# Kernel tuning notes

Hardware: AMD Instinct MI355X
Metric: run time of the kernel (lower is better)

Reference implementation:

```python
import jax, jax.numpy as jnp
import numpy as np

N_MAPS = 6          # n: maps per class (5 kernels + 1 text)
N_CLASSES = 2       # len(text_classify)
RATIO = 3
LAMBDA = 0.7
EPS = 1e-4
NEG_INF = -1e30


def setup_inputs() -> dict:
    key = jax.random.key(0)
    k1, k2, k3 = jax.random.split(key, 3)
    B, C, H, W = 8, N_CLASSES * N_MAPS, 640, 640
    outputs = jax.random.normal(k1, (B, C, H, W), dtype=jnp.float32)
    labels = jax.random.uniform(k2, (B, C, H, W), dtype=jnp.float32)
    training_mask = jax.random.uniform(k3, (B, 1, H, W), dtype=jnp.float32)
    return {"outputs": outputs, "labels": labels, "training_mask": training_mask}


def _dice_loss(pred, target, mask):
    # pred/target: (B, HW) or (B, K, HW); mask broadcastable. sums over last axis.
    p = jax.nn.sigmoid(pred) * mask
    t = target * mask
    a = jnp.sum(p * t, axis=-1)
    b = jnp.sum(p * p, axis=-1) + EPS
    c = jnp.sum(t * t, axis=-1) + EPS
    return 1.0 - 2.0 * a / (b + c)


def _ohem_single(score, gt, tm):
    # score/gt/tm: (H, W). Returns float32 (H, W) selection mask.
    pos_num = jnp.sum((gt > 0.5) & (tm > 0.5))
    neg = gt <= 0.5
    neg_total = jnp.sum(neg)
    neg_num = jnp.minimum(pos_num * RATIO, neg_total)
    # descending sort of negative-position scores
    neg_sorted = -jnp.sort(-jnp.where(neg, score, NEG_INF).ravel())
    thr = neg_sorted[jnp.clip(neg_num - 1, 0, score.size - 1)]
    sel = ((score >= thr) | (gt > 0.5)) & (tm > 0.5)
    fallback = (pos_num == 0) | (neg_num == 0)
    return jnp.where(fallback, tm, sel.astype(jnp.float32))


def reference(outputs, labels, training_mask):
    B, C, H, W = outputs.shape
    tm = training_mask[:, 0]  # (B, H, W)
    text_losses, kernel_losses, class_losses = [], [], []
    for i in range(N_CLASSES):
        texts = outputs[:, (i + 1) * N_MAPS - 1]                 # (B, H, W)
        kernels = outputs[:, i * N_MAPS:(i + 1) * N_MAPS - 1]    # (B, K, H, W)
        gt_texts = labels[:, (i + 1) * N_MAPS - 1]
        gt_kernels = labels[:, i * N_MAPS:(i + 1) * N_MAPS - 1]
        # OHEM mask (detached in original via numpy round-trip)
        sel_text = jax.lax.stop_gradient(jax.vmap(_ohem_single)(texts, gt_texts, tm))
        loss_text = _dice_loss(texts.reshape(B, -1), gt_texts.reshape(B, -1),
                               sel_text.reshape(B, -1))  # (B,)
        # kernel mask: (sigmoid(texts) > 0.5) & (tm > 0.5), detached
        sel_k = jax.lax.stop_gradient(
            ((jax.nn.sigmoid(texts) > 0.5) & (tm > 0.5)).astype(jnp.float32))
        K = gt_kernels.shape[1]
        loss_kernels = _dice_loss(kernels.reshape(B, K, -1),
                                  gt_kernels.reshape(B, K, -1),
                                  sel_k.reshape(B, 1, -1))  # (B, K) per-kernel losses
        loss_kernels = jnp.mean(loss_kernels, axis=1)  # mean over kernels -> (B,)
        lt = jnp.mean(loss_text)      # reduction='mean'
        lk = jnp.mean(loss_kernels)
        loss = LAMBDA * lt + (1.0 - LAMBDA) * lk
        text_losses.append(lt)
        kernel_losses.append(lk)
        class_losses.append(loss)
    muti_class_loss_avg = jnp.mean(jnp.stack(class_losses))
    text_loss_avg = jnp.mean(jnp.stack(text_losses))
    kernel_loss_avg = jnp.mean(jnp.stack(kernel_losses))
    # stacked as (3,): [muti_class_loss_avg, text_loss_avg, kernel_loss_avg]
    return jnp.stack([muti_class_loss_avg, text_loss_avg, kernel_loss_avg])
```

## Files before the change

### kernel.cpp

```cpp
#include <hip/hip_runtime.h>
#include <hip/hip_cooperative_groups.h>
namespace cg = cooperative_groups;

#define HW 409600
#define NCH 12

#define OFF_TACC   0
#define OFF_KACC   256
#define OFF_TFAST  1280
#define OFF_TFB    1536
#define OFF_POSF   1792
#define OFF_NEGF   1856
#define OFF_DONE   1920
#define OFF_NEGNUM 1984
#define OFF_SEL1   2048
#define OFF_KREM1  2112
#define OFF_SEL2   2176
#define OFF_KREM2  2240
#define OFF_THR    2304
#define OFF_ANYG   2368
#define OFF_HA     4096
#define OFF_HB     (OFF_HA + 16*2048*4)
#define OFF_HC     (OFF_HB + 16*2048*4)

__device__ __forceinline__ unsigned flipkey(float x){
  unsigned b = __float_as_uint(x);
  return (b & 0x80000000u) ? ~b : (b | 0x80000000u);
}
__device__ __forceinline__ float unflip(unsigned u){
  unsigned b = (u & 0x80000000u) ? (u ^ 0x80000000u) : ~u;
  return __uint_as_float(b);
}
__device__ __forceinline__ float sigm(float x){
  return __fdividef(1.0f, 1.0f + __expf(-x));
}

__global__ __launch_bounds__(256) void k_main(
    const float* __restrict__ outputs, const float* __restrict__ labels,
    const float* __restrict__ tmask,
    float* __restrict__ posF, float* __restrict__ negF,
    float* __restrict__ tfastA, float* __restrict__ tfbA,
    float* __restrict__ kaccA)
{
  int img = blockIdx.x / 400;
  int blk = blockIdx.x % 400;
  int ci = img >> 3, bi = img & 7;
  const float* ob = outputs + (size_t)(bi*NCH + ci*6)*HW;
  const float* lb = labels  + (size_t)(bi*NCH + ci*6)*HW;
  const float* mp = tmask   + (size_t)bi*HW;
  int px = blk*1024 + (int)threadIdx.x*4;

  float4 ov0 = *(const float4*)(ob + 0*HW + px);
  float4 ov1 = *(const float4*)(ob + 1*HW + px);
  float4 ov2 = *(const float4*)(ob + 2*HW + px);
  float4 ov3 = *(const float4*)(ob + 3*HW + px);
  float4 ov4 = *(const float4*)(ob + 4*HW + px);
  float4 ov5 = *(const float4*)(ob + 5*HW + px);
  float4 lv0 = *(const float4*)(lb + 0*HW + px);
  float4 lv1 = *(const float4*)(lb + 1*HW + px);
  float4 lv2 = *(const float4*)(lb + 2*HW + px);
  float4 lv3 = *(const float4*)(lb + 3*HW + px);
  float4 lv4 = *(const float4*)(lb + 4*HW + px);
  float4 lv5 = *(const float4*)(lb + 5*HW + px);
  float4 mv  = *(const float4*)(mp + px);

  float oo[6][4] = {{ov0.x,ov0.y,ov0.z,ov0.w},{ov1.x,ov1.y,ov1.z,ov1.w},
                    {ov2.x,ov2.y,ov2.z,ov2.w},{ov3.x,ov3.y,ov3.z,ov3.w},
                    {ov4.x,ov4.y,ov4.z,ov4.w},{ov5.x,ov5.y,ov5.z,ov5.w}};
  float ll[6][4] = {{lv0.x,lv0.y,lv0.z,lv0.w},{lv1.x,lv1.y,lv1.z,lv1.w},
                    {lv2.x,lv2.y,lv2.z,lv2.w},{lv3.x,lv3.y,lv3.z,lv3.w},
                    {lv4.x,lv4.y,lv4.z,lv4.w},{lv5.x,lv5.y,lv5.z,lv5.w}};
  float tmv[4] = {mv.x,mv.y,mv.z,mv.w};

  float ka0=0,ka1=0,ka2=0,ka3=0,ka4=0;
  float kb0=0,kb1=0,kb2=0,kb3=0,kb4=0;
  float kc0=0,kc1=0,kc2=0,kc3=0,kc4=0;
  float af=0,bf=0,cf=0;
  float ab_=0,bb_=0,cb_=0;
  unsigned pos=0, neg=0;

  #pragma unroll
  for (int c=0;c<4;c++){
    float t  = oo[5][c];
    float g  = ll[5][c];
    float tm = tmv[c];
    bool tpos  = (tm > 0.5f);
    bool isneg = (g <= 0.5f);
    bool selk  = (t > 0.0f) && tpos;
    pos += (unsigned)((!isneg) && tpos);
    neg += (unsigned)isneg;

    float s5 = sigm(t);
    float mf = tpos ? 1.0f : 0.0f;
    af += mf * (s5*g);
    bf += mf * (s5*s5);
    cf += mf * (g*g);
    float pfb = s5*tm, tfb = g*tm;
    ab_ += pfb*tfb; bb_ += pfb*pfb; cb_ += tfb*tfb;
    float mk = selk ? 1.0f : 0.0f;
    {
      float s, l;
      s = sigm(oo[0][c]); l = ll[0][c];
      ka0 += mk*(s*l); kb0 += mk*(s*s); kc0 += mk*(l*l);
      s = sigm(oo[1][c]); l = ll[1][c];
      ka1 += mk*(s*l); kb1 += mk*(s*s); kc1 += mk*(l*l);
      s = sigm(oo[2][c]); l = ll[2][c];
      ka2 += mk*(s*l); kb2 += mk*(s*s); kc2 += mk*(l*l);
      s = sigm(oo[3][c]); l = ll[3][c];
      ka3 += mk*(s*l); kb3 += mk*(s*s); kc3 += mk*(l*l);
      s = sigm(oo[4][c]); l = ll[4][c];
      ka4 += mk*(s*l); kb4 += mk*(s*s); kc4 += mk*(l*l);
    }
  }

  float red[23] = {af,bf,cf, ab_,bb_,cb_,
                   ka0,kb0,kc0, ka1,kb1,kc1, ka2,kb2,kc2,
                   ka3,kb3,kc3, ka4,kb4,kc4,
                   (float)pos, (float)neg};
  #pragma unroll
  for (int k=0;k<23;k++){
    #pragma unroll
    for (int o=32;o;o>>=1) red[k] += __shfl_down(red[k],o,64);
  }
  __shared__ float sred[4][23];
  int wv = threadIdx.x >> 6, ln = threadIdx.x & 63;
  if (ln==0){
    #pragma unroll
    for (int k=0;k<23;k++) sred[wv][k] = red[k];
  }
  __syncthreads();
  int t = threadIdx.x;
  if (t < 23){
    float v = sred[0][t]+sred[1][t]+sred[2][t]+sred[3][t];
    float* dst;
    if      (t < 3)  dst = tfastA + img*3 + t;
    else if (t < 6)  dst = tfbA   + img*3 + (t-3);
    else if (t < 21) dst = kaccA  + img*15 + (t-6);
    else if (t ==21) dst = posF + img;
    else             dst = negF + img;
    atomicAdd(dst, v);
  }
}

template<int NB>
__device__ void scan_desc(const unsigned* h, unsigned k, unsigned* selOut, unsigned* kremOut)
{
  const int PER = NB/256;
  int t = threadIdx.x;
  unsigned s=0;
  #pragma unroll
  for (int j=0;j<PER;j++) s += h[t*PER+j];
  __shared__ unsigned cs[256];
  cs[t]=s; __syncthreads();
  if (t==0){
    unsigned cum=0, ch=0, kin=k;
    for (int c=255;c>=0;c--){
      if (cum + cs[c] >= k){ ch=(unsigned)c; kin=k-cum; break; }
      cum += cs[c];
    }
    unsigned cum2=0, sel=ch*PER, kr=1;
    for (int x=PER-1;x>=0;x--){
      unsigned v = h[ch*PER+x];
      cum2 += v;
      if (cum2 >= kin){ sel=ch*PER+(unsigned)x; kr = kin - (cum2 - v); break; }
    }
    *selOut = sel; *kremOut = kr;
  }
  __syncthreads();
}

__device__ void do_final(const float* tacc, const float* kacc, float* out)
{
  const float EPSF = 1e-4f;
  float ltA[2], lkA[2];
  for (int i=0;i<2;i++){
    float lt=0.f;
    for (int b=0;b<8;b++){
      int img=i*8+b;
      float a=tacc[img*3], p2=tacc[img*3+1]+EPSF, t2=tacc[img*3+2]+EPSF;
      lt += 1.f - 2.f*a/(p2+t2);
    }
    lt *= 0.125f;
    float lk=0.f;
    for (int b=0;b<8;b++) for (int k=0;k<5;k++){
      int idx=((i*8+b)*5+k)*3;
      float a=kacc[idx], p2=kacc[idx+1]+EPSF, t2=kacc[idx+2]+EPSF;
      lk += 1.f - 2.f*a/(p2+t2);
    }
    lk /= 40.f;
    ltA[i]=lt; lkA[i]=lk;
  }
  float l0 = 0.7f*ltA[0] + 0.3f*lkA[0];
  float l1 = 0.7f*ltA[1] + 0.3f*lkA[1];
  out[0]=0.5f*(l0+l1);
  out[1]=0.5f*(ltA[0]+ltA[1]);
  out[2]=0.5f*(lkA[0]+lkA[1]);
}

__global__ __launch_bounds__(256) void k_tail(
    const float* __restrict__ outputs, const float* __restrict__ labels,
    const float* __restrict__ tmask, char* __restrict__ ws, float* __restrict__ out)
{
  cg::grid_group grid = cg::this_grid();
  float* tacc      = (float*)(ws + OFF_TACC);
  float* kacc      = (float*)(ws + OFF_KACC);
  float* tfastA    = (float*)(ws + OFF_TFAST);
  float* tfbA      = (float*)(ws + OFF_TFB);
  float* posF      = (float*)(ws + OFF_POSF);
  float* negF      = (float*)(ws + OFF_NEGF);
  unsigned* doneA  = (unsigned*)(ws + OFF_DONE);
  unsigned* negnumA= (unsigned*)(ws + OFF_NEGNUM);
  unsigned* sel1A  = (unsigned*)(ws + OFF_SEL1);
  unsigned* krem1A = (unsigned*)(ws + OFF_KREM1);
  unsigned* sel2A  = (unsigned*)(ws + OFF_SEL2);
  unsigned* krem2A = (unsigned*)(ws + OFF_KREM2);
  float* thrA      = (float*)(ws + OFF_THR);
  unsigned* anyG   = (unsigned*)(ws + OFF_ANYG);
  unsigned* histA  = (unsigned*)(ws + OFF_HA);
  unsigned* histB  = (unsigned*)(ws + OFF_HB);
  unsigned* histC  = (unsigned*)(ws + OFF_HC);

  if (blockIdx.x == 0){
    int t = threadIdx.x;
    unsigned d = 1u;
    if (t < 16){
      float pos = posF[t], negt = negF[t];
      float nn = fminf(pos*3.0f, negt);
      bool fb   = (pos == 0.0f) || (nn == 0.0f);
      bool fast = (!fb) && (nn == negt);
      d = (fb || fast) ? 1u : 0u;
      doneA[t] = d;
      negnumA[t] = d ? 1u : (unsigned)(nn + 0.5f);
      thrA[t] = 0.0f;
      if (d){
        const float* src = fb ? (tfbA + t*3) : (tfastA + t*3);
        tacc[t*3+0] = src[0];
        tacc[t*3+1] = src[1];
        tacc[t*3+2] = src[2];
      }
    }
    unsigned long long nd = __ballot((t < 16) && (d == 0u));
    if (t == 0) anyG[0] = (nd != 0ull) ? 1u : 0u;
    __threadfence();
  }
  grid.sync();

  if (anyG[0] == 0u){
    if (blockIdx.x == 0 && threadIdx.x == 0) do_final(tacc, kacc, out);
    return;
  }

  for (int i = blockIdx.x*256 + threadIdx.x; i < 81920; i += gridDim.x*256)
    histA[i] = 0u;
  grid.sync();

  __shared__ unsigned lh[2048];

  for (int tile = blockIdx.x; tile < 800; tile += gridDim.x){
    int img = tile/50;
    if (doneA[img]) continue;
    int blk = tile%50;
    int ci = img>>3, bi = img&7;
    const float* tp = outputs + (size_t)(bi*NCH + ci*6 + 5)*HW;
    const float* gp = labels  + (size_t)(bi*NCH + ci*6 + 5)*HW;
    for (int j=threadIdx.x; j<2048; j+=256) lh[j]=0u;
    __syncthreads();
    for (int it=0; it<8; it++){
      int px = blk*8192 + it*1024 + (int)threadIdx.x*4;
      float4 tv = *(const float4*)(tp+px);
      float4 gv = *(const float4*)(gp+px);
      float tt[4]={tv.x,tv.y,tv.z,tv.w};
      float gg[4]={gv.x,gv.y,gv.z,gv.w};
      #pragma unroll
      for (int c=0;c<4;c++)
        if (gg[c] <= 0.5f) atomicAdd(&lh[flipkey(tt[c]) >> 21], 1u);
    }
    __syncthreads();
    unsigned* gh = histA + (size_t)img*2048u;
    for (int j=threadIdx.x; j<2048; j+=256){
      unsigned v = lh[j];
      if (v) atomicAdd(&gh[j], v);
    }
    __syncthreads();
  }
  grid.sync();

  if (blockIdx.x < 16 && !doneA[blockIdx.x])
    scan_desc<2048>(histA + (size_t)blockIdx.x*2048u, negnumA[blockIdx.x],
                    &sel1A[blockIdx.x], &krem1A[blockIdx.x]);
  grid.sync();

  for (int tile = blockIdx.x; tile < 800; tile += gridDim.x){
    int img = tile/50;
    if (doneA[img]) continue;
    int blk = tile%50;
    int ci = img>>3, bi = img&7;
    unsigned sel1 = sel1A[img];
    const float* tp = outputs + (size_t)(bi*NCH + ci*6 + 5)*HW;
    const float* gp = labels  + (size_t)(bi*NCH + ci*6 + 5)*HW;
    for (int j=threadIdx.x; j<2048; j+=256) lh[j]=0u;
    __syncthreads();
    for (int it=0; it<8; it++){
      int px = blk*8192 + it*1024 + (int)threadIdx.x*4;
      float4 tv = *(const float4*)(tp+px);
      float4 gv = *(const float4*)(gp+px);
      float tt[4]={tv.x,tv.y,tv.z,tv.w};
      float gg[4]={gv.x,gv.y,gv.z,gv.w};
      #pragma unroll
      for (int c=0;c<4;c++){
        if (gg[c] <= 0.5f){
          unsigned key = flipkey(tt[c]);
          if ((key>>21) == sel1) atomicAdd(&lh[(key>>10) & 0x7FFu], 1u);
        }
      }
    }
    __syncthreads();
    unsigned* gh = histB + (size_t)img*2048u;
    for (int j=threadIdx.x; j<2048; j+=256){
      unsigned v = lh[j];
      if (v) atomicAdd(&gh[j], v);
    }
    __syncthreads();
  }
  grid.sync();

  if (blockIdx.x < 16 && !doneA[blockIdx.x])
    scan_desc<2048>(histB + (size_t)blockIdx.x*2048u, krem1A[blockIdx.x],
                    &sel2A[blockIdx.x], &krem2A[blockIdx.x]);
  grid.sync();

  for (int tile = blockIdx.x; tile < 800; tile += gridDim.x){
    int img = tile/50;
    if (doneA[img]) continue;
    int blk = tile%50;
    int ci = img>>3, bi = img&7;
    unsigned p22 = (sel1A[img]<<11) | sel2A[img];
    const float* tp = outputs + (size_t)(bi*NCH + ci*6 + 5)*HW;
    const float* gp = labels  + (size_t)(bi*NCH + ci*6 + 5)*HW;
    for (int j=threadIdx.x; j<1024; j+=256) lh[j]=0u;
    __syncthreads();
    for (int it=0; it<8; it++){
      int px = blk*8192 + it*1024 + (int)threadIdx.x*4;
      float4 tv = *(const float4*)(tp+px);
      float4 gv = *(const float4*)(gp+px);
      float tt[4]={tv.x,tv.y,tv.z,tv.w};
      float gg[4]={gv.x,gv.y,gv.z,gv.w};
      #pragma unroll
      for (int c=0;c<4;c++){
        if (gg[c] <= 0.5f){
          unsigned key = flipkey(tt[c]);
          if ((key>>10) == p22) atomicAdd(&lh[key & 0x3FFu], 1u);
        }
      }
    }
    __syncthreads();
    unsigned* gh = histC + (size_t)img*1024u;
    for (int j=threadIdx.x; j<1024; j+=256){
      unsigned v = lh[j];
      if (v) atomicAdd(&gh[j], v);
    }
    __syncthreads();
  }
  grid.sync();

  if (blockIdx.x < 16 && !doneA[blockIdx.x]){
    __shared__ unsigned sel3, kr;
    scan_desc<1024>(histC + (size_t)blockIdx.x*1024u, krem2A[blockIdx.x], &sel3, &kr);
    if (threadIdx.x==0){
      unsigned key = (sel1A[blockIdx.x]<<21) | (sel2A[blockIdx.x]<<10) | sel3;
      thrA[blockIdx.x] = unflip(key);
    }
  }
  grid.sync();

  for (int tile = blockIdx.x; tile < 800; tile += gridDim.x){
    int img = tile/50;
    if (doneA[img]) continue;
    int blk = tile%50;
    int ci = img>>3, bi = img&7;
    const float* tp = outputs + (size_t)(bi*NCH + ci*6 + 5)*HW;
    const float* gp = labels  + (size_t)(bi*NCH + ci*6 + 5)*HW;
    const float* mp = tmask   + (size_t)bi*HW;
    float thr = thrA[img];
    float sa=0.f, sb=0.f, sc=0.f;
    for (int it=0; it<8; it++){
      int px = blk*8192 + it*1024 + (int)threadIdx.x*4;
      float4 pv = *(const float4*)(tp+px);
      float4 gv = *(const float4*)(gp+px);
      float4 mv = *(const float4*)(mp+px);
      float pa[4]={pv.x,pv.y,pv.z,pv.w};
      float ga[4]={gv.x,gv.y,gv.z,gv.w};
      float ma[4]={mv.x,mv.y,mv.z,mv.w};
      #pragma unroll
      for (int c=0;c<4;c++){
        float m = (((pa[c] >= thr) || (ga[c] > 0.5f)) && (ma[c] > 0.5f)) ? 1.0f : 0.0f;
        float p = sigm(pa[c]) * m;
        float tt = ga[c]*m;
        sa += p*tt; sb += p*p; sc += tt*tt;
      }
    }
    #pragma unroll
    for (int o=32;o;o>>=1){
      sa += __shfl_down(sa,o,64); sb += __shfl_down(sb,o,64); sc += __shfl_down(sc,o,64);
    }
    __shared__ float ra[4], rb[4], rc[4];
    int wv = threadIdx.x>>6, ln = threadIdx.x&63;
    if (ln==0){ ra[wv]=sa; rb[wv]=sb; rc[wv]=sc; }
    __syncthreads();
    if (threadIdx.x==0){
      float* acc = tacc + img*3;
      atomicAdd(acc+0, ra[0]+ra[1]+ra[2]+ra[3]);
      atomicAdd(acc+1, rb[0]+rb[1]+rb[2]+rb[3]);
      atomicAdd(acc+2, rc[0]+rc[1]+rc[2]+rc[3]);
    }
    __syncthreads();
  }
  grid.sync();

  if (blockIdx.x == 0 && threadIdx.x == 0) do_final(tacc, kacc, out);
}

extern "C" void kernel_launch(void* const* d_in, const int* in_sizes, int n_in,
                              void* d_out, int out_size, void* d_ws, size_t ws_size,
                              hipStream_t stream)
{
  const float* outputs = (const float*)d_in[0];
  const float* labels  = (const float*)d_in[1];
  const float* tmask   = (const float*)d_in[2];
  float* out = (float*)d_out;
  char* ws = (char*)d_ws;
  float* posF      = (float*)(ws + OFF_POSF);
  float* negF      = (float*)(ws + OFF_NEGF);
  float* tfastA    = (float*)(ws + OFF_TFAST);
  float* tfbA      = (float*)(ws + OFF_TFB);
  float* kacc      = (float*)(ws + OFF_KACC);

  hipMemsetAsync(ws, 0, 2048, stream);
  k_main<<<6400,256,0,stream>>>(outputs, labels, tmask, posF, negF,
                                tfastA, tfbA, kacc);
  void* args[] = { (void*)&outputs, (void*)&labels, (void*)&tmask,
                   (void*)&ws, (void*)&out };
  hipLaunchCooperativeKernel((const void*)k_tail, dim3(256), dim3(256),
                             args, 0, stream);
}
```

Baseline: 392.9 us.

## Replace cooperative grid-synced tail with per-image block and partial-slot reduction

```diff
diff --git a/kernel.cpp b/kernel.cpp
--- a/kernel.cpp
+++ b/kernel.cpp
@@ -1,27 +1,12 @@
 #include <hip/hip_runtime.h>
-#include <hip/hip_cooperative_groups.h>
-namespace cg = cooperative_groups;
 
 #define HW 409600
 #define NCH 12
 
-#define OFF_TACC   0
-#define OFF_KACC   256
-#define OFF_TFAST  1280
-#define OFF_TFB    1536
-#define OFF_POSF   1792
-#define OFF_NEGF   1856
-#define OFF_DONE   1920
-#define OFF_NEGNUM 1984
-#define OFF_SEL1   2048
-#define OFF_KREM1  2112
-#define OFF_SEL2   2176
-#define OFF_KREM2  2240
-#define OFF_THR    2304
-#define OFF_ANYG   2368
-#define OFF_HA     4096
-#define OFF_HB     (OFF_HA + 16*2048*4)
-#define OFF_HC     (OFF_HB + 16*2048*4)
+#define OFF_PSLOT  0
+#define OFF_TACC   294912
+#define OFF_KACC   295168
+#define OFF_CNT    296192
 
 __device__ __forceinline__ unsigned flipkey(float x){
   unsigned b = __float_as_uint(x);
@@ -37,40 +22,16 @@
 
 __global__ __launch_bounds__(256) void k_main(
     const float* __restrict__ outputs, const float* __restrict__ labels,
-    const float* __restrict__ tmask,
-    float* __restrict__ posF, float* __restrict__ negF,
-    float* __restrict__ tfastA, float* __restrict__ tfbA,
-    float* __restrict__ kaccA)
-{
-  int img = blockIdx.x / 400;
-  int blk = blockIdx.x % 400;
+    const float* __restrict__ tmask, float* __restrict__ pslot,
+    unsigned* __restrict__ cnt)
+{
+  if (blockIdx.x == 0 && threadIdx.x == 0) *cnt = 0u;
+  int img = blockIdx.x / 200;
+  int blk = blockIdx.x % 200;
   int ci = img >> 3, bi = img & 7;
   const float* ob = outputs + (size_t)(bi*NCH + ci*6)*HW;
   const float* lb = labels  + (size_t)(bi*NCH + ci*6)*HW;
   const float* mp = tmask   + (size_t)bi*HW;
-  int px = blk*1024 + (int)threadIdx.x*4;
-
-  float4 ov0 = *(const float4*)(ob + 0*HW + px);
-  float4 ov1 = *(const float4*)(ob + 1*HW + px);
-  float4 ov2 = *(const float4*)(ob + 2*HW + px);
-  float4 ov3 = *(const float4*)(ob + 3*HW + px);
-  float4 ov4 = *(const float4*)(ob + 4*HW + px);
-  float4 ov5 = *(const float4*)(ob + 5*HW + px);
-  float4 lv0 = *(const float4*)(lb + 0*HW + px);
-  float4 lv1 = *(const float4*)(lb + 1*HW + px);
-  float4 lv2 = *(const float4*)(lb + 2*HW + px);
-  float4 lv3 = *(const float4*)(lb + 3*HW + px);
-  float4 lv4 = *(const float4*)(lb + 4*HW + px);
-  float4 lv5 = *(const float4*)(lb + 5*HW + px);
-  float4 mv  = *(const float4*)(mp + px);
-
-  float oo[6][4] = {{ov0.x,ov0.y,ov0.z,ov0.w},{ov1.x,ov1.y,ov1.z,ov1.w},
-                    {ov2.x,ov2.y,ov2.z,ov2.w},{ov3.x,ov3.y,ov3.z,ov3.w},
-                    {ov4.x,ov4.y,ov4.z,ov4.w},{ov5.x,ov5.y,ov5.z,ov5.w}};
-  float ll[6][4] = {{lv0.x,lv0.y,lv0.z,lv0.w},{lv1.x,lv1.y,lv1.z,lv1.w},
-                    {lv2.x,lv2.y,lv2.z,lv2.w},{lv3.x,lv3.y,lv3.z,lv3.w},
-                    {lv4.x,lv4.y,lv4.z,lv4.w},{lv5.x,lv5.y,lv5.z,lv5.w}};
-  float tmv[4] = {mv.x,mv.y,mv.z,mv.w};
 
   float ka0=0,ka1=0,ka2=0,ka3=0,ka4=0;
   float kb0=0,kb1=0,kb2=0,kb3=0,kb4=0;
@@ -80,36 +41,62 @@
   unsigned pos=0, neg=0;
 
   #pragma unroll
-  for (int c=0;c<4;c++){
-    float t  = oo[5][c];
-    float g  = ll[5][c];
-    float tm = tmv[c];
-    bool tpos  = (tm > 0.5f);
-    bool isneg = (g <= 0.5f);
-    bool selk  = (t > 0.0f) && tpos;
-    pos += (unsigned)((!isneg) && tpos);
-    neg += (unsigned)isneg;
-
-    float s5 = sigm(t);
-    float mf = tpos ? 1.0f : 0.0f;
-    af += mf * (s5*g);
-    bf += mf * (s5*s5);
-    cf += mf * (g*g);
-    float pfb = s5*tm, tfb = g*tm;
-    ab_ += pfb*tfb; bb_ += pfb*pfb; cb_ += tfb*tfb;
-    float mk = selk ? 1.0f : 0.0f;
-    {
-      float s, l;
-      s = sigm(oo[0][c]); l = ll[0][c];
-      ka0 += mk*(s*l); kb0 += mk*(s*s); kc0 += mk*(l*l);
-      s = sigm(oo[1][c]); l = ll[1][c];
-      ka1 += mk*(s*l); kb1 += mk*(s*s); kc1 += mk*(l*l);
-      s = sigm(oo[2][c]); l = ll[2][c];
-      ka2 += mk*(s*l); kb2 += mk*(s*s); kc2 += mk*(l*l);
-      s = sigm(oo[3][c]); l = ll[3][c];
-      ka3 += mk*(s*l); kb3 += mk*(s*s); kc3 += mk*(l*l);
-      s = sigm(oo[4][c]); l = ll[4][c];
-      ka4 += mk*(s*l); kb4 += mk*(s*s); kc4 += mk*(l*l);
+  for (int it=0; it<2; it++){
+    int px = blk*2048 + it*1024 + (int)threadIdx.x*4;
+    float4 ov0 = *(const float4*)(ob + 0*HW + px);
+    float4 ov1 = *(const float4*)(ob + 1*HW + px);
+    float4 ov2 = *(const float4*)(ob + 2*HW + px);
+    float4 ov3 = *(const float4*)(ob + 3*HW + px);
+    float4 ov4 = *(const float4*)(ob + 4*HW + px);
+    float4 ov5 = *(const float4*)(ob + 5*HW + px);
+    float4 lv0 = *(const float4*)(lb + 0*HW + px);
+    float4 lv1 = *(const float4*)(lb + 1*HW + px);
+    float4 lv2 = *(const float4*)(lb + 2*HW + px);
+    float4 lv3 = *(const float4*)(lb + 3*HW + px);
+    float4 lv4 = *(const float4*)(lb + 4*HW + px);
+    float4 lv5 = *(const float4*)(lb + 5*HW + px);
+    float4 mv  = *(const float4*)(mp + px);
+
+    float oo[6][4] = {{ov0.x,ov0.y,ov0.z,ov0.w},{ov1.x,ov1.y,ov1.z,ov1.w},
+                      {ov2.x,ov2.y,ov2.z,ov2.w},{ov3.x,ov3.y,ov3.z,ov3.w},
+                      {ov4.x,ov4.y,ov4.z,ov4.w},{ov5.x,ov5.y,ov5.z,ov5.w}};
+    float ll[6][4] = {{lv0.x,lv0.y,lv0.z,lv0.w},{lv1.x,lv1.y,lv1.z,lv1.w},
+                      {lv2.x,lv2.y,lv2.z,lv2.w},{lv3.x,lv3.y,lv3.z,lv3.w},
+                      {lv4.x,lv4.y,lv4.z,lv4.w},{lv5.x,lv5.y,lv5.z,lv5.w}};
+    float tmv[4] = {mv.x,mv.y,mv.z,mv.w};
+
+    #pragma unroll
+    for (int c=0;c<4;c++){
+      float t  = oo[5][c];
+      float g  = ll[5][c];
+      float tm = tmv[c];
+      bool tpos  = (tm > 0.5f);
+      bool isneg = (g <= 0.5f);
+      bool selk  = (t > 0.0f) && tpos;
+      pos += (unsigned)((!isneg) && tpos);
+      neg += (unsigned)isneg;
+
+      float s5 = sigm(t);
+      float mf = tpos ? 1.0f : 0.0f;
+      af += mf * (s5*g);
+      bf += mf * (s5*s5);
+      cf += mf * (g*g);
+      float pfb = s5*tm, tfb = g*tm;
+      ab_ += pfb*tfb; bb_ += pfb*pfb; cb_ += tfb*tfb;
+      float mk = selk ? 1.0f : 0.0f;
+      {
+        float s, l;
+        s = sigm(oo[0][c]); l = ll[0][c];
+        ka0 += mk*(s*l); kb0 += mk*(s*s); kc0 += mk*(l*l);
+        s = sigm(oo[1][c]); l = ll[1][c];
+        ka1 += mk*(s*l); kb1 += mk*(s*s); kc1 += mk*(l*l);
+        s = sigm(oo[2][c]); l = ll[2][c];
+        ka2 += mk*(s*l); kb2 += mk*(s*s); kc2 += mk*(l*l);
+        s = sigm(oo[3][c]); l = ll[3][c];
+        ka3 += mk*(s*l); kb3 += mk*(s*s); kc3 += mk*(l*l);
+        s = sigm(oo[4][c]); l = ll[4][c];
+        ka4 += mk*(s*l); kb4 += mk*(s*s); kc4 += mk*(l*l);
+      }
     }
   }
 
@@ -130,16 +117,8 @@
   }
   __syncthreads();
   int t = threadIdx.x;
-  if (t < 23){
-    float v = sred[0][t]+sred[1][t]+sred[2][t]+sred[3][t];
-    float* dst;
-    if      (t < 3)  dst = tfastA + img*3 + t;
-    else if (t < 6)  dst = tfbA   + img*3 + (t-3);
-    else if (t < 21) dst = kaccA  + img*15 + (t-6);
-    else if (t ==21) dst = posF + img;
-    else             dst = negF + img;
-    atomicAdd(dst, v);
-  }
+  if (t < 23)
+    pslot[(size_t)blockIdx.x*23 + t] = sred[0][t]+sred[1][t]+sred[2][t]+sred[3][t];
 }
 
 template<int NB>
@@ -201,190 +180,114 @@
     const float* __restrict__ outputs, const float* __restrict__ labels,
     const float* __restrict__ tmask, char* __restrict__ ws, float* __restrict__ out)
 {
-  cg::grid_group grid = cg::this_grid();
-  float* tacc      = (float*)(ws + OFF_TACC);
-  float* kacc      = (float*)(ws + OFF_KACC);
-  float* tfastA    = (float*)(ws + OFF_TFAST);
-  float* tfbA      = (float*)(ws + OFF_TFB);
-  float* posF      = (float*)(ws + OFF_POSF);
-  float* negF      = (float*)(ws + OFF_NEGF);
-  unsigned* doneA  = (unsigned*)(ws + OFF_DONE);
-  unsigned* negnumA= (unsigned*)(ws + OFF_NEGNUM);
-  unsigned* sel1A  = (unsigned*)(ws + OFF_SEL1);
-  unsigned* krem1A = (unsigned*)(ws + OFF_KREM1);
-  unsigned* sel2A  = (unsigned*)(ws + OFF_SEL2);
-  unsigned* krem2A = (unsigned*)(ws + OFF_KREM2);
-  float* thrA      = (float*)(ws + OFF_THR);
-  unsigned* anyG   = (unsigned*)(ws + OFF_ANYG);
-  unsigned* histA  = (unsigned*)(ws + OFF_HA);
-  unsigned* histB  = (unsigned*)(ws + OFF_HB);
-  unsigned* histC  = (unsigned*)(ws + OFF_HC);
-
-  if (blockIdx.x == 0){
-    int t = threadIdx.x;
-    unsigned d = 1u;
-    if (t < 16){
-      float pos = posF[t], negt = negF[t];
-      float nn = fminf(pos*3.0f, negt);
-      bool fb   = (pos == 0.0f) || (nn == 0.0f);
-      bool fast = (!fb) && (nn == negt);
-      d = (fb || fast) ? 1u : 0u;
-      doneA[t] = d;
-      negnumA[t] = d ? 1u : (unsigned)(nn + 0.5f);
-      thrA[t] = 0.0f;
-      if (d){
-        const float* src = fb ? (tfbA + t*3) : (tfastA + t*3);
-        tacc[t*3+0] = src[0];
-        tacc[t*3+1] = src[1];
-        tacc[t*3+2] = src[2];
-      }
-    }
-    unsigned long long nd = __ballot((t < 16) && (d == 0u));
-    if (t == 0) anyG[0] = (nd != 0ull) ? 1u : 0u;
-    __threadfence();
-  }
-  grid.sync();
-
-  if (anyG[0] == 0u){
-    if (blockIdx.x == 0 && threadIdx.x == 0) do_final(tacc, kacc, out);
-    return;
-  }
-
-  for (int i = blockIdx.x*256 + threadIdx.x; i < 81920; i += gridDim.x*256)
-    histA[i] = 0u;
-  grid.sync();
-
-  __shared__ unsigned lh[2048];
-
-  for (int tile = blockIdx.x; tile < 800; tile += gridDim.x){
-    int img = tile/50;
-    if (doneA[img]) continue;
-    int blk = tile%50;
-    int ci = img>>3, bi = img&7;
+  float* pslot = (float*)(ws + OFF_PSLOT);
+  float* tacc  = (float*)(ws + OFF_TACC);
+  float* kacc  = (float*)(ws + OFF_KACC);
+  unsigned* cnt= (unsigned*)(ws + OFF_CNT);
+  int img = blockIdx.x;
+  int t = threadIdx.x;
+  int ci = img>>3, bi = img&7;
+
+  const float* ps = pslot + (size_t)img*200*23;
+  __shared__ float part[8][23];
+  __shared__ float rsum[23];
+  int g = t/23, c = t - g*23;
+  if (g < 8){
+    float s = 0.f;
+    for (int r=g; r<200; r+=8) s += ps[r*23 + c];
+    part[g][c] = s;
+  }
+  __syncthreads();
+  if (t < 23){
+    float s = 0.f;
+    #pragma unroll
+    for (int q=0;q<8;q++) s += part[q][t];
+    rsum[t] = s;
+  }
+  __syncthreads();
+
+  if (t >= 6 && t < 21) kacc[img*15 + (t-6)] = rsum[t];
+
+  __shared__ unsigned smode;
+  __shared__ unsigned snegnum;
+  if (t==0){
+    float pos = rsum[21], negt = rsum[22];
+    float nn = fminf(pos*3.0f, negt);
+    bool fb   = (pos == 0.0f) || (nn == 0.0f);
+    bool fast = (!fb) && (nn == negt);
+    smode = fb ? 2u : (fast ? 1u : 0u);
+    snegnum = (unsigned)(nn + 0.5f);
+  }
+  __syncthreads();
+  unsigned mode = smode;
+
+  if (mode){
+    if (t < 3) tacc[img*3 + t] = rsum[(mode==2u ? 3 : 0) + t];
+  } else {
     const float* tp = outputs + (size_t)(bi*NCH + ci*6 + 5)*HW;
     const float* gp = labels  + (size_t)(bi*NCH + ci*6 + 5)*HW;
-    for (int j=threadIdx.x; j<2048; j+=256) lh[j]=0u;
-    __syncthreads();
-    for (int it=0; it<8; it++){
-      int px = blk*8192 + it*1024 + (int)threadIdx.x*4;
+    const float* mp = tmask   + (size_t)bi*HW;
+    __shared__ unsigned lh[2048];
+    __shared__ unsigned sel1, krem1, sel2, krem2, sel3, krem3;
+
+    for (int j=t; j<2048; j+=256) lh[j]=0u;
+    __syncthreads();
+    for (int px=t*4; px<HW; px+=1024){
       float4 tv = *(const float4*)(tp+px);
       float4 gv = *(const float4*)(gp+px);
       float tt[4]={tv.x,tv.y,tv.z,tv.w};
       float gg[4]={gv.x,gv.y,gv.z,gv.w};
       #pragma unroll
-      for (int c=0;c<4;c++)
-        if (gg[c] <= 0.5f) atomicAdd(&lh[flipkey(tt[c]) >> 21], 1u);
-    }
-    __syncthreads();
-    unsigned* gh = histA + (size_t)img*2048u;
-    for (int j=threadIdx.x; j<2048; j+=256){
-      unsigned v = lh[j];
-      if (v) atomicAdd(&gh[j], v);
-    }
-    __syncthreads();
-  }
-  grid.sync();
-
-  if (blockIdx.x < 16 && !doneA[blockIdx.x])
-    scan_desc<2048>(histA + (size_t)blockIdx.x*2048u, negnumA[blockIdx.x],
-                    &sel1A[blockIdx.x], &krem1A[blockIdx.x]);
-  grid.sync();
-
-  for (int tile = blockIdx.x; tile < 800; tile += gridDim.x){
-    int img = tile/50;
-    if (doneA[img]) continue;
-    int blk = tile%50;
-    int ci = img>>3, bi = img&7;
-    unsigned sel1 = sel1A[img];
-    const float* tp = outputs + (size_t)(bi*NCH + ci*6 + 5)*HW;
-    const float* gp = labels  + (size_t)(bi*NCH + ci*6 + 5)*HW;
-    for (int j=threadIdx.x; j<2048; j+=256) lh[j]=0u;
-    __syncthreads();
-    for (int it=0; it<8; it++){
-      int px = blk*8192 + it*1024 + (int)threadIdx.x*4;
+      for (int k=0;k<4;k++)
+        if (gg[k] <= 0.5f) atomicAdd(&lh[flipkey(tt[k]) >> 21], 1u);
+    }
+    __syncthreads();
+    scan_desc<2048>(lh, snegnum, &sel1, &krem1);
+
+    unsigned s1 = sel1;
+    unsigned k1 = krem1;
+    for (int j=t; j<2048; j+=256) lh[j]=0u;
+    __syncthreads();
+    for (int px=t*4; px<HW; px+=1024){
       float4 tv = *(const float4*)(tp+px);
       float4 gv = *(const float4*)(gp+px);
       float tt[4]={tv.x,tv.y,tv.z,tv.w};
       float gg[4]={gv.x,gv.y,gv.z,gv.w};
       #pragma unroll
-      for (int c=0;c<4;c++){
-        if (gg[c] <= 0.5f){
-          unsigned key = flipkey(tt[c]);
-          if ((key>>21) == sel1) atomicAdd(&lh[(key>>10) & 0x7FFu], 1u);
+      for (int k=0;k<4;k++){
+        if (gg[k] <= 0.5f){
+          unsigned key = flipkey(tt[k]);
+          if ((key>>21) == s1) atomicAdd(&lh[(key>>10) & 0x7FFu], 1u);
         }
       }
     }
     __syncthreads();
-    unsigned* gh = histB + (size_t)img*2048u;
-    for (int j=threadIdx.x; j<2048; j+=256){
-      unsigned v = lh[j];
-      if (v) atomicAdd(&gh[j], v);
-    }
-    __syncthreads();
-  }
-  grid.sync();
-
-  if (blockIdx.x < 16 && !doneA[blockIdx.x])
-    scan_desc<2048>(histB + (size_t)blockIdx.x*2048u, krem1A[blockIdx.x],
-                    &sel2A[blockIdx.x], &krem2A[blockIdx.x]);
-  grid.sync();
-
-  for (int tile = blockIdx.x; tile < 800; tile += gridDim.x){
-    int img = tile/50;
-    if (doneA[img]) continue;
-    int blk = tile%50;
-    int ci = img>>3, bi = img&7;
-    unsigned p22 = (sel1A[img]<<11) | sel2A[img];
-    const float* tp = outputs + (size_t)(bi*NCH + ci*6 + 5)*HW;
-    const float* gp = labels  + (size_t)(bi*NCH + ci*6 + 5)*HW;
-    for (int j=threadIdx.x; j<1024; j+=256) lh[j]=0u;
-    __syncthreads();
-    for (int it=0; it<8; it++){
-      int px = blk*8192 + it*1024 + (int)threadIdx.x*4;
+    scan_desc<2048>(lh, k1, &sel2, &krem2);
+
+    unsigned p22 = (s1<<11) | sel2;
+    unsigned k2 = krem2;
+    for (int j=t; j<1024; j+=256) lh[j]=0u;
+    __syncthreads();
+    for (int px=t*4; px<HW; px+=1024){
       float4 tv = *(const float4*)(tp+px);
       float4 gv = *(const float4*)(gp+px);
       float tt[4]={tv.x,tv.y,tv.z,tv.w};
       float gg[4]={gv.x,gv.y,gv.z,gv.w};
       #pragma unroll
-      for (int c=0;c<4;c++){
-        if (gg[c] <= 0.5f){
-          unsigned key = flipkey(tt[c]);
+      for (int k=0;k<4;k++){
+        if (gg[k] <= 0.5f){
+          unsigned key = flipkey(tt[k]);
           if ((key>>10) == p22) atomicAdd(&lh[key & 0x3FFu], 1u);
         }
       }
     }
     __syncthreads();
-    unsigned* gh = histC + (size_t)img*1024u;
-    for (int j=threadIdx.x; j<1024; j+=256){
-      unsigned v = lh[j];
-      if (v) atomicAdd(&gh[j], v);
-    }
-    __syncthreads();
-  }
-  grid.sync();
-
-  if (blockIdx.x < 16 && !doneA[blockIdx.x]){
-    __shared__ unsigned sel3, kr;
-    scan_desc<1024>(histC + (size_t)blockIdx.x*1024u, krem2A[blockIdx.x], &sel3, &kr);
-    if (threadIdx.x==0){
-      unsigned key = (sel1A[blockIdx.x]<<21) | (sel2A[blockIdx.x]<<10) | sel3;
-      thrA[blockIdx.x] = unflip(key);
-    }
-  }
-  grid.sync();
-
-  for (int tile = blockIdx.x; tile < 800; tile += gridDim.x){
-    int img = tile/50;
-    if (doneA[img]) continue;
-    int blk = tile%50;
-    int ci = img>>3, bi = img&7;
-    const float* tp = outputs + (size_t)(bi*NCH + ci*6 + 5)*HW;
-    const float* gp = labels  + (size_t)(bi*NCH + ci*6 + 5)*HW;
-    const float* mp = tmask   + (size_t)bi*HW;
-    float thr = thrA[img];
+    scan_desc<1024>(lh, k2, &sel3, &krem3);
+
+    float thr = unflip((s1<<21) | (sel2<<10) | sel3);
+
     float sa=0.f, sb=0.f, sc=0.f;
-    for (int it=0; it<8; it++){
-      int px = blk*8192 + it*1024 + (int)threadIdx.x*4;
+    for (int px=t*4; px<HW; px+=1024){
       float4 pv = *(const float4*)(tp+px);
       float4 gv = *(const float4*)(gp+px);
       float4 mv = *(const float4*)(mp+px);
@@ -392,10 +295,10 @@
       float ga[4]={gv.x,gv.y,gv.z,gv.w};
       float ma[4]={mv.x,mv.y,mv.z,mv.w};
       #pragma unroll
-      for (int c=0;c<4;c++){
-        float m = (((pa[c] >= thr) || (ga[c] > 0.5f)) && (ma[c] > 0.5f)) ? 1.0f : 0.0f;
-        float p = sigm(pa[c]) * m;
-        float tt = ga[c]*m;
+      for (int k=0;k<4;k++){
+        float m = (((pa[k] >= thr) || (ga[k] > 0.5f)) && (ma[k] > 0.5f)) ? 1.0f : 0.0f;
+        float p = sigm(pa[k]) * m;
+        float tt = ga[k]*m;
         sa += p*tt; sb += p*p; sc += tt*tt;
       }
     }
@@ -404,20 +307,24 @@
       sa += __shfl_down(sa,o,64); sb += __shfl_down(sb,o,64); sc += __shfl_down(sc,o,64);
     }
     __shared__ float ra[4], rb[4], rc[4];
-    int wv = threadIdx.x>>6, ln = threadIdx.x&63;
+    int wv = t>>6, ln = t&63;
     if (ln==0){ ra[wv]=sa; rb[wv]=sb; rc[wv]=sc; }
     __syncthreads();
-    if (threadIdx.x==0){
-      float* acc = tacc + img*3;
-      atomicAdd(acc+0, ra[0]+ra[1]+ra[2]+ra[3]);
-      atomicAdd(acc+1, rb[0]+rb[1]+rb[2]+rb[3]);
-      atomicAdd(acc+2, rc[0]+rc[1]+rc[2]+rc[3]);
-    }
-    __syncthreads();
-  }
-  grid.sync();
-
-  if (blockIdx.x == 0 && threadIdx.x == 0) do_final(tacc, kacc, out);
+    if (t==0){
+      tacc[img*3+0] = ra[0]+ra[1]+ra[2]+ra[3];
+      tacc[img*3+1] = rb[0]+rb[1]+rb[2]+rb[3];
+      tacc[img*3+2] = rc[0]+rc[1]+rc[2]+rc[3];
+    }
+  }
+
+  __threadfence();
+  __syncthreads();
+  if (t==0) atomicAdd(cnt, 1u);
+  if (img==0 && t==0){
+    while (atomicAdd(cnt, 0u) < 16u) { __builtin_amdgcn_s_sleep(8); }
+    __threadfence();
+    do_final(tacc, kacc, out);
+  }
 }
 
 extern "C" void kernel_launch(void* const* d_in, const int* in_sizes, int n_in,
@@ -429,17 +336,9 @@
   const float* tmask   = (const float*)d_in[2];
   float* out = (float*)d_out;
   char* ws = (char*)d_ws;
-  float* posF      = (float*)(ws + OFF_POSF);
-  float* negF      = (float*)(ws + OFF_NEGF);
-  float* tfastA    = (float*)(ws + OFF_TFAST);
-  float* tfbA      = (float*)(ws + OFF_TFB);
-  float* kacc      = (float*)(ws + OFF_KACC);
-
-  hipMemsetAsync(ws, 0, 2048, stream);
-  k_main<<<6400,256,0,stream>>>(outputs, labels, tmask, posF, negF,
-                                tfastA, tfbA, kacc);
-  void* args[] = { (void*)&outputs, (void*)&labels, (void*)&tmask,
-                   (void*)&ws, (void*)&out };
-  hipLaunchCooperativeKernel((const void*)k_tail, dim3(256), dim3(256),
-                             args, 0, stream);
-}
+  float* pslot  = (float*)(ws + OFF_PSLOT);
+  unsigned* cnt = (unsigned*)(ws + OFF_CNT);
+
+  k_main<<<3200,256,0,stream>>>(outputs, labels, tmask, pslot, cnt);
+  k_tail<<<16,256,0,stream>>>(outputs, labels, tmask, ws, out);
+}
```

Result: faster. 346.5 us (-11.8%).
